# Kernel optimization log

Hardware: AMD Instinct MI355X
Metric: run time of the kernel (lower is better)

## Reference

```python
import jax, jax.numpy as jnp
import numpy as np

V = 45      # vocab / input_size / output_size
H = 2048    # hidden_size
W = 128     # stack_width
D = 200     # stack_depth


def setup_inputs() -> dict:
    key = jax.random.key(0)
    ks = jax.random.split(key, 14)
    s = 0.02
    return {
        "inp": jax.random.randint(ks[0], (1,), 0, V),
        "hidden": jax.random.normal(ks[1], (1, 1, H), jnp.float32),
        "stack": jax.random.normal(ks[2], (1, D, W), jnp.float32),
        "emb": jax.random.normal(ks[3], (V, H), jnp.float32) * s,
        "ctrl_W": jax.random.normal(ks[4], (3, H), jnp.float32) * s,
        "ctrl_b": jnp.zeros((3,), jnp.float32),
        "sin_W": jax.random.normal(ks[5], (W, H), jnp.float32) * s,
        "sin_b": jnp.zeros((W,), jnp.float32),
        "w_ih": jax.random.normal(ks[6], (3 * H, H + W), jnp.float32) * s,
        "w_hh": jax.random.normal(ks[7], (3 * H, H), jnp.float32) * s,
        "b_ih": jnp.zeros((3 * H,), jnp.float32),
        "b_hh": jnp.zeros((3 * H,), jnp.float32),
        "dec_W": jax.random.normal(ks[8], (V, H), jnp.float32) * s,
        "dec_b": jnp.zeros((V,), jnp.float32),
    }


def reference(inp, hidden, stack, emb, ctrl_W, ctrl_b, sin_W, sin_b,
              w_ih, w_hh, b_ih, b_hh, dec_W, dec_b):
    h = hidden[0]  # [1, H]  (n_layers=1, unidirectional -> squeeze(0))

    # --- differentiable stack update ---
    controls = jax.nn.softmax(h @ ctrl_W.T + ctrl_b, axis=1)      # [1, 3]
    stack_input = jnp.tanh(h @ sin_W.T + sin_b)[:, None, :]       # [1, 1, W]
    zeros_bottom = jnp.zeros((1, 1, W), stack.dtype)
    stack_down = jnp.concatenate([stack[:, 1:], zeros_bottom], axis=1)   # pop
    stack_up = jnp.concatenate([stack_input, stack[:, :-1]], axis=1)    # push
    c = controls.reshape(1, 3, 1, 1)  # (push, pop, no_op)
    new_stack = c[:, 2] * stack + c[:, 0] * stack_up + c[:, 1] * stack_down
    stack_top = new_stack[:, 0, :]  # [1, W]

    # --- embed token, concat stack top ---
    x = jnp.concatenate([emb[inp].reshape(1, -1), stack_top], axis=1)  # [1, H+W]

    # --- GRU cell (PyTorch gate convention) ---
    gi = x @ w_ih.T + b_ih   # [1, 3H]
    gh = h @ w_hh.T + b_hh   # [1, 3H]
    i_r, i_z, i_n = jnp.split(gi, 3, axis=1)
    h_r, h_z, h_n = jnp.split(gh, 3, axis=1)
    r = jax.nn.sigmoid(i_r + h_r)
    z = jax.nn.sigmoid(i_z + h_z)
    n = jnp.tanh(i_n + r * h_n)
    h_new = (1.0 - z) * n + z * h   # [1, H]

    # --- decoder ---
    output = h_new @ dec_W.T + dec_b  # [1, V]
    return output, h_new[None], new_stack
```

## Files before the change

### kernel.cpp

```cpp
#include <hip/hip_runtime.h>
#include <hip/hip_bf16.h>

#define V_SZ 45
#define H_SZ 2048
#define W_SZ 128
#define D_SZ 200
#define X_SZ (H_SZ + W_SZ)

#define WS_CTRL 0
#define WS_SIN  16
#define WS_X    160
#define WS_HNEW 2432

__device__ __forceinline__ float dot4(float4 a, float4 b) {
  return a.x * b.x + a.y * b.y + a.z * b.z + a.w * b.w;
}

__device__ __forceinline__ float wave_reduce(float v) {
#pragma unroll
  for (int o = 32; o > 0; o >>= 1) v += __shfl_down(v, o, 64);
  return v;
}

__global__ __launch_bounds__(256) void k1_small_gemv(
    const float* __restrict__ hidden,
    const float* __restrict__ ctrl_W,
    const float* __restrict__ ctrl_b,
    const float* __restrict__ sin_W,
    const float* __restrict__ sin_b,
    float* __restrict__ ws) {
  const int b = blockIdx.x;
  const int tid = threadIdx.x;
  const float* row = (b < 3) ? (ctrl_W + (size_t)b * H_SZ)
                             : (sin_W + (size_t)(b - 3) * H_SZ);
  const float4* rw4 = (const float4*)row;
  const float4* rh4 = (const float4*)hidden;
  float acc = dot4(rw4[tid], rh4[tid]) + dot4(rw4[tid + 256], rh4[tid + 256]);

  acc = wave_reduce(acc);
  __shared__ float red[4];
  const int wv_id = tid >> 6;
  if ((tid & 63) == 0) red[wv_id] = acc;
  __syncthreads();
  if (tid == 0) {
    float total = red[0] + red[1] + red[2] + red[3];
    if (b < 3) {
      ws[WS_CTRL + b] = total + ctrl_b[b];
    } else {
      ws[WS_SIN + (b - 3)] = tanhf(total + sin_b[b - 3]);
    }
  }
}

__global__ __launch_bounds__(256) void k2_stack(
    const int* __restrict__ inp,
    const float* __restrict__ stack,
    const float* __restrict__ emb,
    float* __restrict__ ws,
    float* __restrict__ out) {
  const int i = blockIdx.x * 256 + threadIdx.x;
  const float l0 = ws[WS_CTRL + 0], l1 = ws[WS_CTRL + 1], l2 = ws[WS_CTRL + 2];
  const float m = fmaxf(l0, fmaxf(l1, l2));
  const float e0 = expf(l0 - m), e1 = expf(l1 - m), e2 = expf(l2 - m);
  const float inv = 1.f / (e0 + e1 + e2);
  const float c0 = e0 * inv, c1 = e1 * inv, c2 = e2 * inv;

  if (i < D_SZ * W_SZ) {
    const int d = i >> 7;
    const int w = i & (W_SZ - 1);
    const float s = stack[i];
    const float up = (d == 0) ? ws[WS_SIN + w] : stack[i - W_SZ];
    const float dn = (d == D_SZ - 1) ? 0.f : stack[i + W_SZ];
    const float ns = c2 * s + c0 * up + c1 * dn;
    out[V_SZ + H_SZ + i] = ns;
    if (d == 0) ws[WS_X + H_SZ + w] = ns;
  } else if (i < D_SZ * W_SZ + H_SZ) {
    const int k = i - D_SZ * W_SZ;
    const int idx = inp[0];
    ws[WS_X + k] = emb[(size_t)idx * H_SZ + k];
  }
}

__global__ __launch_bounds__(256) void k3_gru(
    const float* __restrict__ hidden,
    const float* __restrict__ w_ih,
    const float* __restrict__ w_hh,
    const float* __restrict__ b_ih,
    const float* __restrict__ b_hh,
    float* __restrict__ ws,
    float* __restrict__ out) {
  __shared__ __align__(16) float xs[X_SZ];
  __shared__ __align__(16) float hs[H_SZ];
  __shared__ float red[4][6];
  const int tid = threadIdx.x;
  const int j = blockIdx.x;

  for (int k = tid; k < X_SZ; k += 256) xs[k] = ws[WS_X + k];
  for (int k = tid; k < H_SZ; k += 256) hs[k] = hidden[k];
  __syncthreads();

  float a0 = 0.f, a1 = 0.f, a2 = 0.f, a3 = 0.f, a4 = 0.f, a5 = 0.f;

  const float4* wi0 = (const float4*)(w_ih + (size_t)j * X_SZ);
  const float4* wi1 = (const float4*)(w_ih + (size_t)(j + H_SZ) * X_SZ);
  const float4* wi2 = (const float4*)(w_ih + (size_t)(j + 2 * H_SZ) * X_SZ);
  const float4* xs4 = (const float4*)xs;
  for (int c = tid; c < X_SZ / 4; c += 256) {
    const float4 xv = xs4[c];
    a0 += dot4(wi0[c], xv);
    a1 += dot4(wi1[c], xv);
    a2 += dot4(wi2[c], xv);
  }

  const float4* wh0 = (const float4*)(w_hh + (size_t)j * H_SZ);
  const float4* wh1 = (const float4*)(w_hh + (size_t)(j + H_SZ) * H_SZ);
  const float4* wh2 = (const float4*)(w_hh + (size_t)(j + 2 * H_SZ) * H_SZ);
  const float4* hs4 = (const float4*)hs;
#pragma unroll
  for (int q = 0; q < 2; ++q) {
    const int c = tid + q * 256;
    const float4 hv = hs4[c];
    a3 += dot4(wh0[c], hv);
    a4 += dot4(wh1[c], hv);
    a5 += dot4(wh2[c], hv);
  }

  a0 = wave_reduce(a0); a1 = wave_reduce(a1); a2 = wave_reduce(a2);
  a3 = wave_reduce(a3); a4 = wave_reduce(a4); a5 = wave_reduce(a5);
  const int wv_id = tid >> 6;
  if ((tid & 63) == 0) {
    red[wv_id][0] = a0; red[wv_id][1] = a1; red[wv_id][2] = a2;
    red[wv_id][3] = a3; red[wv_id][4] = a4; red[wv_id][5] = a5;
  }
  __syncthreads();
  if (tid == 0) {
    float t[6];
#pragma unroll
    for (int q = 0; q < 6; ++q)
      t[q] = red[0][q] + red[1][q] + red[2][q] + red[3][q];
    const float gi_r = t[0] + b_ih[j];
    const float gi_z = t[1] + b_ih[j + H_SZ];
    const float gi_n = t[2] + b_ih[j + 2 * H_SZ];
    const float gh_r = t[3] + b_hh[j];
    const float gh_z = t[4] + b_hh[j + H_SZ];
    const float gh_n = t[5] + b_hh[j + 2 * H_SZ];
    const float r = 1.f / (1.f + expf(-(gi_r + gh_r)));
    const float z = 1.f / (1.f + expf(-(gi_z + gh_z)));
    const float n = tanhf(gi_n + r * gh_n);
    const float hn = (1.f - z) * n + z * hs[j];
    ws[WS_HNEW + j] = hn;
    out[V_SZ + j] = hn;
  }
}

__global__ __launch_bounds__(256) void k4_dec(
    const float* __restrict__ dec_W,
    const float* __restrict__ dec_b,
    const float* __restrict__ hnew,
    float* __restrict__ out) {
  const int v = blockIdx.x;
  const int tid = threadIdx.x;
  const float4* row = (const float4*)(dec_W + (size_t)v * H_SZ);
  const float4* h4 = (const float4*)hnew;
  float acc = dot4(row[tid], h4[tid]) + dot4(row[tid + 256], h4[tid + 256]);

  acc = wave_reduce(acc);
  __shared__ float red[4];
  const int wv_id = tid >> 6;
  if ((tid & 63) == 0) red[wv_id] = acc;
  __syncthreads();
  if (tid == 0) {
    out[v] = red[0] + red[1] + red[2] + red[3] + dec_b[v];
  }
}

extern "C" void kernel_launch(void* const* d_in, const int* in_sizes, int n_in,
                              void* d_out, int out_size, void* d_ws, size_t ws_size,
                              hipStream_t stream) {
  const int*   inp    = (const int*)d_in[0];
  const float* hidden = (const float*)d_in[1];
  const float* stack  = (const float*)d_in[2];
  const float* emb    = (const float*)d_in[3];
  const float* ctrl_W = (const float*)d_in[4];
  const float* ctrl_b = (const float*)d_in[5];
  const float* sin_W  = (const float*)d_in[6];
  const float* sin_b  = (const float*)d_in[7];
  const float* w_ih   = (const float*)d_in[8];
  const float* w_hh   = (const float*)d_in[9];
  const float* b_ih   = (const float*)d_in[10];
  const float* b_hh   = (const float*)d_in[11];
  const float* dec_W  = (const float*)d_in[12];
  const float* dec_b  = (const float*)d_in[13];
  float* out = (float*)d_out;
  float* ws = (float*)d_ws;

  k1_small_gemv<<<3 + W_SZ, 256, 0, stream>>>(hidden, ctrl_W, ctrl_b, sin_W, sin_b, ws);
  k2_stack<<<(D_SZ * W_SZ + H_SZ) / 256, 256, 0, stream>>>(inp, stack, emb, ws, out);
  k3_gru<<<H_SZ, 256, 0, stream>>>(hidden, w_ih, w_hh, b_ih, b_hh, ws, out);
  k4_dec<<<V_SZ, 256, 0, stream>>>(dec_W, dec_b, ws + WS_HNEW, out);
}
```

Before: 155.9 us.

## Fuse stack update into GRU and decoder kernels, drop staging kernel

Removes the separate stack/embedding staging kernel. The GRU kernel now reads the embedding row directly and computes the new stack top inline from the control softmax. The full stack update is moved into the decoder launch as extra blocks. The GRU kernel also drops its shared-memory staging of x and h and reads them straight from global memory. Fast __expf replaces expf. This saves one launch and a workspace round trip, at the cost of redundant softmax work in every block.

```diff
diff --git a/kernel.cpp b/kernel.cpp
--- a/kernel.cpp
+++ b/kernel.cpp
@@ -9,8 +9,7 @@
 
 #define WS_CTRL 0
 #define WS_SIN  16
-#define WS_X    160
-#define WS_HNEW 2432
+#define WS_HNEW 160
 
 __device__ __forceinline__ float dot4(float4 a, float4 b) {
   return a.x * b.x + a.y * b.y + a.z * b.z + a.w * b.w;
@@ -20,6 +19,15 @@
 #pragma unroll
   for (int o = 32; o > 0; o >>= 1) v += __shfl_down(v, o, 64);
   return v;
+}
+
+__device__ __forceinline__ void ctrl_softmax(const float* __restrict__ ws,
+                                             float& c0, float& c1, float& c2) {
+  const float l0 = ws[WS_CTRL + 0], l1 = ws[WS_CTRL + 1], l2 = ws[WS_CTRL + 2];
+  const float m = fmaxf(l0, fmaxf(l1, l2));
+  const float e0 = __expf(l0 - m), e1 = __expf(l1 - m), e2 = __expf(l2 - m);
+  const float inv = 1.f / (e0 + e1 + e2);
+  c0 = e0 * inv; c1 = e1 * inv; c2 = e2 * inv;
 }
 
 __global__ __launch_bounds__(256) void k1_small_gemv(
@@ -52,74 +60,61 @@
   }
 }
 
-__global__ __launch_bounds__(256) void k2_stack(
+__global__ __launch_bounds__(256) void k3_gru(
     const int* __restrict__ inp,
+    const float* __restrict__ hidden,
+    const float* __restrict__ emb,
     const float* __restrict__ stack,
-    const float* __restrict__ emb,
-    float* __restrict__ ws,
-    float* __restrict__ out) {
-  const int i = blockIdx.x * 256 + threadIdx.x;
-  const float l0 = ws[WS_CTRL + 0], l1 = ws[WS_CTRL + 1], l2 = ws[WS_CTRL + 2];
-  const float m = fmaxf(l0, fmaxf(l1, l2));
-  const float e0 = expf(l0 - m), e1 = expf(l1 - m), e2 = expf(l2 - m);
-  const float inv = 1.f / (e0 + e1 + e2);
-  const float c0 = e0 * inv, c1 = e1 * inv, c2 = e2 * inv;
-
-  if (i < D_SZ * W_SZ) {
-    const int d = i >> 7;
-    const int w = i & (W_SZ - 1);
-    const float s = stack[i];
-    const float up = (d == 0) ? ws[WS_SIN + w] : stack[i - W_SZ];
-    const float dn = (d == D_SZ - 1) ? 0.f : stack[i + W_SZ];
-    const float ns = c2 * s + c0 * up + c1 * dn;
-    out[V_SZ + H_SZ + i] = ns;
-    if (d == 0) ws[WS_X + H_SZ + w] = ns;
-  } else if (i < D_SZ * W_SZ + H_SZ) {
-    const int k = i - D_SZ * W_SZ;
-    const int idx = inp[0];
-    ws[WS_X + k] = emb[(size_t)idx * H_SZ + k];
-  }
-}
-
-__global__ __launch_bounds__(256) void k3_gru(
-    const float* __restrict__ hidden,
     const float* __restrict__ w_ih,
     const float* __restrict__ w_hh,
     const float* __restrict__ b_ih,
     const float* __restrict__ b_hh,
     float* __restrict__ ws,
     float* __restrict__ out) {
-  __shared__ __align__(16) float xs[X_SZ];
-  __shared__ __align__(16) float hs[H_SZ];
-  __shared__ float red[4][6];
   const int tid = threadIdx.x;
   const int j = blockIdx.x;
-
-  for (int k = tid; k < X_SZ; k += 256) xs[k] = ws[WS_X + k];
-  for (int k = tid; k < H_SZ; k += 256) hs[k] = hidden[k];
-  __syncthreads();
 
   float a0 = 0.f, a1 = 0.f, a2 = 0.f, a3 = 0.f, a4 = 0.f, a5 = 0.f;
 
   const float4* wi0 = (const float4*)(w_ih + (size_t)j * X_SZ);
   const float4* wi1 = (const float4*)(w_ih + (size_t)(j + H_SZ) * X_SZ);
   const float4* wi2 = (const float4*)(w_ih + (size_t)(j + 2 * H_SZ) * X_SZ);
-  const float4* xs4 = (const float4*)xs;
-  for (int c = tid; c < X_SZ / 4; c += 256) {
-    const float4 xv = xs4[c];
+  const float4* emb4 = (const float4*)(emb + (size_t)inp[0] * H_SZ);
+
+#pragma unroll
+  for (int q = 0; q < 2; ++q) {
+    const int c = tid + q * 256;
+    const float4 xv = emb4[c];
     a0 += dot4(wi0[c], xv);
     a1 += dot4(wi1[c], xv);
     a2 += dot4(wi2[c], xv);
   }
+  if (tid < (X_SZ - H_SZ) / 4) {
+    const int c = 512 + tid;
+    const int w = 4 * tid;
+    float c0, c1, c2;
+    ctrl_softmax(ws, c0, c1, c2);
+    const float4 s0 = *(const float4*)(stack + w);
+    const float4 s1 = *(const float4*)(stack + W_SZ + w);
+    const float4 sv = *(const float4*)(ws + WS_SIN + w);
+    float4 xv;
+    xv.x = c2 * s0.x + c0 * sv.x + c1 * s1.x;
+    xv.y = c2 * s0.y + c0 * sv.y + c1 * s1.y;
+    xv.z = c2 * s0.z + c0 * sv.z + c1 * s1.z;
+    xv.w = c2 * s0.w + c0 * sv.w + c1 * s1.w;
+    a0 += dot4(wi0[c], xv);
+    a1 += dot4(wi1[c], xv);
+    a2 += dot4(wi2[c], xv);
+  }
 
   const float4* wh0 = (const float4*)(w_hh + (size_t)j * H_SZ);
   const float4* wh1 = (const float4*)(w_hh + (size_t)(j + H_SZ) * H_SZ);
   const float4* wh2 = (const float4*)(w_hh + (size_t)(j + 2 * H_SZ) * H_SZ);
-  const float4* hs4 = (const float4*)hs;
+  const float4* h4 = (const float4*)hidden;
 #pragma unroll
   for (int q = 0; q < 2; ++q) {
     const int c = tid + q * 256;
-    const float4 hv = hs4[c];
+    const float4 hv = h4[c];
     a3 += dot4(wh0[c], hv);
     a4 += dot4(wh1[c], hv);
     a5 += dot4(wh2[c], hv);
@@ -127,6 +122,7 @@
 
   a0 = wave_reduce(a0); a1 = wave_reduce(a1); a2 = wave_reduce(a2);
   a3 = wave_reduce(a3); a4 = wave_reduce(a4); a5 = wave_reduce(a5);
+  __shared__ float red[4][6];
   const int wv_id = tid >> 6;
   if ((tid & 63) == 0) {
     red[wv_id][0] = a0; red[wv_id][1] = a1; red[wv_id][2] = a2;
@@ -144,33 +140,43 @@
     const float gh_r = t[3] + b_hh[j];
     const float gh_z = t[4] + b_hh[j + H_SZ];
     const float gh_n = t[5] + b_hh[j + 2 * H_SZ];
-    const float r = 1.f / (1.f + expf(-(gi_r + gh_r)));
-    const float z = 1.f / (1.f + expf(-(gi_z + gh_z)));
+    const float r = 1.f / (1.f + __expf(-(gi_r + gh_r)));
+    const float z = 1.f / (1.f + __expf(-(gi_z + gh_z)));
     const float n = tanhf(gi_n + r * gh_n);
-    const float hn = (1.f - z) * n + z * hs[j];
+    const float hn = (1.f - z) * n + z * hidden[j];
     ws[WS_HNEW + j] = hn;
     out[V_SZ + j] = hn;
   }
 }
 
-__global__ __launch_bounds__(256) void k4_dec(
+__global__ __launch_bounds__(256) void k4_dec_stack(
     const float* __restrict__ dec_W,
     const float* __restrict__ dec_b,
-    const float* __restrict__ hnew,
+    const float* __restrict__ stack,
+    float* __restrict__ ws,
     float* __restrict__ out) {
-  const int v = blockIdx.x;
   const int tid = threadIdx.x;
-  const float4* row = (const float4*)(dec_W + (size_t)v * H_SZ);
-  const float4* h4 = (const float4*)hnew;
-  float acc = dot4(row[tid], h4[tid]) + dot4(row[tid + 256], h4[tid + 256]);
-
-  acc = wave_reduce(acc);
-  __shared__ float red[4];
-  const int wv_id = tid >> 6;
-  if ((tid & 63) == 0) red[wv_id] = acc;
-  __syncthreads();
-  if (tid == 0) {
-    out[v] = red[0] + red[1] + red[2] + red[3] + dec_b[v];
+  if (blockIdx.x < V_SZ) {
+    const int v = blockIdx.x;
+    const float4* row = (const float4*)(dec_W + (size_t)v * H_SZ);
+    const float4* h4 = (const float4*)(ws + WS_HNEW);
+    float acc = dot4(row[tid], h4[tid]) + dot4(row[tid + 256], h4[tid + 256]);
+    acc = wave_reduce(acc);
+    __shared__ float red[4];
+    const int wv_id = tid >> 6;
+    if ((tid & 63) == 0) red[wv_id] = acc;
+    __syncthreads();
+    if (tid == 0) out[v] = red[0] + red[1] + red[2] + red[3] + dec_b[v];
+  } else {
+    const int i = (blockIdx.x - V_SZ) * 256 + tid;
+    float c0, c1, c2;
+    ctrl_softmax(ws, c0, c1, c2);
+    const int d = i >> 7;
+    const int w = i & (W_SZ - 1);
+    const float s = stack[i];
+    const float up = (d == 0) ? ws[WS_SIN + w] : stack[i - W_SZ];
+    const float dn = (d == D_SZ - 1) ? 0.f : stack[i + W_SZ];
+    out[V_SZ + H_SZ + i] = c2 * s + c0 * up + c1 * dn;
   }
 }
 
@@ -195,7 +201,6 @@
   float* ws = (float*)d_ws;
 
   k1_small_gemv<<<3 + W_SZ, 256, 0, stream>>>(hidden, ctrl_W, ctrl_b, sin_W, sin_b, ws);
-  k2_stack<<<(D_SZ * W_SZ + H_SZ) / 256, 256, 0, stream>>>(inp, stack, emb, ws, out);
-  k3_gru<<<H_SZ, 256, 0, stream>>>(hidden, w_ih, w_hh, b_ih, b_hh, ws, out);
-  k4_dec<<<V_SZ, 256, 0, stream>>>(dec_W, dec_b, ws + WS_HNEW, out);
-}
+  k3_gru<<<H_SZ, 256, 0, stream>>>(inp, hidden, emb, stack, w_ih, w_hh, b_ih, b_hh, ws, out);
+  k4_dec_stack<<<V_SZ + (D_SZ * W_SZ) / 256, 256, 0, stream>>>(dec_W, dec_b, stack, ws, out);
+}
```

New measurement: 153.5 us. Within noise of the previous version (-1.5%).
